# Kernel tuning notes

Measured on AMD Instinct MI355X. Metric: run time of the kernel, lower is better.

Reference implementation:

```python
import jax, jax.numpy as jnp
import numpy as np
import math

B, C, SEG, SEGLEN, K, GROUPS, WG = 8, 256, 40, 200, 10, 32, 4
L4 = SEGLEN // 4            # 50 temporal slots per segment
N = SEG * L4                # 2000 total points
WIDTH = GROUPS * WG         # 128 bottleneck width


def build_neighbor_idx(seg_lens):
    """Exact numpy replication of torch get_temporal_graph's neighbor-list loop.
    Returns flat (into B*N rows) neighbor indices of shape (B, N, 3)."""
    seg_lens = np.asarray(seg_lens)
    Bn, S = seg_lens.shape
    nb = np.zeros((Bn, S * L4, 3), dtype=np.int64)
    for i in range(Bn):
        last_valid = 0
        skip_seg = 0
        base = i * S * L4
        for j in range(S):
            valid = math.ceil(seg_lens[i, j] / 4.0)
            for k in range(L4):
                idx = j * L4 + k
                if k < valid:
                    nb[i, idx] = [base + last_valid, base + idx, base + idx]
                    last_valid = idx
                    if k == 0 and j != 0:
                        nb[i, skip_seg, 2] = base + idx
                    if k == valid - 1:
                        skip_seg = idx
                    else:
                        nb[i, idx, 2] = base + idx + 1
                else:
                    nb[i, idx] = [base + idx] * 3
    return nb


def conv1x1(x, W, b):
    # x: (B, Cin, N, T), W: (Cout, Cin)
    return jnp.einsum('bcnt,oc->bont', x, W) + b[None, :, None, None]


def grouped_1x3(x, W, b):
    # x: (B, WIDTH, N, 3), W: (WIDTH, WIDTH//GROUPS, 3); valid conv -> T_out = 1
    Bn, _, Nn, _ = x.shape
    xg = x.reshape(Bn, GROUPS, WIDTH // GROUPS, Nn, 3)
    Wg = W.reshape(GROUPS, WIDTH // GROUPS, WIDTH // GROUPS, 3)
    y = jnp.einsum('bgcnt,goct->bgon', xg, Wg)
    return y.reshape(Bn, WIDTH, Nn, 1) + b[None, :, None, None]


def grouped_1x1(x, W, b):
    # x: (B, WIDTH, N, T), W: (WIDTH, WIDTH//GROUPS)
    Bn, _, Nn, T = x.shape
    xg = x.reshape(Bn, GROUPS, WIDTH // GROUPS, Nn, T)
    Wg = W.reshape(GROUPS, WIDTH // GROUPS, WIDTH // GROUPS)
    y = jnp.einsum('bgcnt,goc->bgont', xg, Wg)
    return y.reshape(Bn, WIDTH, Nn, T) + b[None, :, None, None]


def setup_inputs() -> dict:
    key = jax.random.key(0)
    ks = jax.random.split(key, 10)
    s = 0.05
    x = jax.random.normal(ks[0], (B, C, N), dtype=jnp.float32)
    seg_lens = jax.random.randint(ks[1], (B, SEG), 0, 201)
    neighbor_idx = jnp.asarray(build_neighbor_idx(np.asarray(seg_lens)))
    return dict(
        x=x, seg_lens=seg_lens, neighbor_idx=neighbor_idx,
        tW1=jax.random.normal(ks[2], (WIDTH, C), jnp.float32) * s,
        tb1=jnp.zeros((WIDTH,), jnp.float32),
        tW2=jax.random.normal(ks[3], (WIDTH, WIDTH // GROUPS, 3), jnp.float32) * s,
        tb2=jnp.zeros((WIDTH,), jnp.float32),
        tW3=jax.random.normal(ks[4], (C, WIDTH), jnp.float32) * s,
        tb3=jnp.zeros((C,), jnp.float32),
        sW1=jax.random.normal(ks[5], (WIDTH, 2 * C), jnp.float32) * s,
        sb1=jnp.zeros((WIDTH,), jnp.float32),
        sW2=jax.random.normal(ks[6], (WIDTH, WIDTH // GROUPS), jnp.float32) * s,
        sb2=jnp.zeros((WIDTH,), jnp.float32),
        sW3=jax.random.normal(ks[7], (C, WIDTH), jnp.float32) * s,
        sb3=jnp.zeros((C,), jnp.float32),
    )


def reference(x, seg_lens, neighbor_idx, tW1, tb1, tW2, tb2, tW3, tb3,
              sW1, sb1, sW2, sb2, sW3, sb3):
    relu = jax.nn.relu
    B_, C_, N_ = x.shape
    flat = x.transpose(0, 2, 1).reshape(B_ * N_, C_)  # (B*N, C)

    # --- temporal branch: gather 3 temporal-graph neighbors -> (B, C, N, 3) ---
    tg = flat[neighbor_idx.reshape(-1)].reshape(B_, N_, 3, C_).transpose(0, 3, 1, 2)
    h = relu(conv1x1(tg, tW1, tb1))
    h = relu(grouped_1x3(h, tW2, tb2))
    tout = conv1x1(h, tW3, tb3).max(axis=-1)  # (B, C, N)

    # --- semantic branch: kNN graph feature (style=1) ---
    xx = jnp.sum(x * x, axis=1)                       # (B, N)
    inner = jnp.einsum('bci,bcj->bij', x, x)          # (B, N, N)
    pd = 2.0 * inner - xx[:, None, :] - xx[:, :, None]  # negative sq. distances
    _, idx = jax.lax.top_k(pd, K)                     # (B, N, K)
    base = (jnp.arange(B_) * N_)[:, None, None]
    nbr = flat[(idx + base).reshape(-1)].reshape(B_, N_, K, C_)
    center = jnp.broadcast_to(x.transpose(0, 2, 1)[:, :, None, :], (B_, N_, K, C_))
    xf = jnp.concatenate([nbr, center], axis=3).transpose(0, 3, 1, 2)  # (B, 2C, N, K)
    g = relu(conv1x1(xf, sW1, sb1))
    g = relu(grouped_1x1(g, sW2, sb2))
    sout = conv1x1(g, sW3, sb3).max(axis=-1)  # (B, C, N)

    return relu(tout + x + sout)
```

## Files before the change

kernel.cpp:

```cpp
#include <hip/hip_runtime.h>

#define NPTS 2000
#define NBATCH 8
#define NC 256
#define NW 128
#define NK 10
#define NROWS (NBATCH * NPTS)
#define JPAD 2048

typedef _Float16 f16x8 __attribute__((ext_vector_type(8)));
typedef _Float16 f16x4 __attribute__((ext_vector_type(4)));
typedef float f32x4 __attribute__((ext_vector_type(4)));

__device__ __forceinline__ float dot4(float4 a, float4 b) {
    return a.x*b.x + a.y*b.y + a.z*b.z + a.w*b.w;
}
__device__ __forceinline__ float4 relu4(float4 a) {
    return make_float4(fmaxf(a.x,0.f), fmaxf(a.y,0.f), fmaxf(a.z,0.f), fmaxf(a.w,0.f));
}
__device__ __forceinline__ float4 add4(float4 a, float4 b) {
    return make_float4(a.x+b.x, a.y+b.y, a.z+b.z, a.w+b.w);
}

__device__ __forceinline__ void ins10(float d, int j, float* vals, int* idxs) {
    if (d > vals[9]) {
        float v = d; int id = j;
        #pragma unroll
        for (int s = 0; s < 10; ++s) {
            if (v > vals[s]) {
                float tv = vals[s]; vals[s] = v; v = tv;
                int   ti = idxs[s]; idxs[s] = id; id = ti;
            }
        }
    }
}

__global__ __launch_bounds__(256) void k_prep(
    const float* __restrict__ x, _Float16* __restrict__ xb,
    float* __restrict__ xx)
{
    __shared__ float T[64][259];
    __shared__ float Pp[64][4];
    const int t  = threadIdx.x;
    const int b  = blockIdx.x >> 5;
    const int n0 = (blockIdx.x & 31) * 64;

    #pragma unroll
    for (int p = 0; p < 64; ++p) {
        const int idx = p*256 + t;
        const int c = idx >> 6, nl = idx & 63;
        T[nl][c] = x[((size_t)b*NC + c)*NPTS + min(n0 + nl, NPTS-1)];
    }
    __syncthreads();

    const int row = t & 63, q = t >> 6;
    const int gr  = n0 + row;
    const bool ok = gr < NPTS;
    const size_t rb = ((size_t)b*JPAD + gr) * 512;
    float ss = 0.f;
    #pragma unroll
    for (int u = 0; u < 2; ++u) {
        const int kc = 2*q + u;
        #pragma unroll
        for (int g = 0; g < 4; ++g) {
            f16x8 vh, vl;
            #pragma unroll
            for (int e = 0; e < 8; ++e) {
                const float f = ok ? T[row][kc*32 + g*8 + e] : 0.f;
                ss = fmaf(f, f, ss);
                const _Float16 h = (_Float16)f;
                vh[e] = h;
                vl[e] = (_Float16)(f - (float)h);
            }
            *(f16x8*)&xb[rb + (kc*2    )*32 + g*8] = vh;
            *(f16x8*)&xb[rb + (kc*2 + 1)*32 + g*8] = vl;
        }
    }
    Pp[row][q] = ss;
    __syncthreads();
    if (t < 64 && n0 + t < NPTS)
        xx[(size_t)b*NPTS + n0 + t] = Pp[t][0] + Pp[t][1] + Pp[t][2] + Pp[t][3];
}

__global__ __launch_bounds__(256) void k_wprep(const float* __restrict__ a,
                                               _Float16* __restrict__ o, int n)
{
    const int i = (blockIdx.x*256 + threadIdx.x)*4;
    if (i < n) {
        const float4 v = *(const float4*)&a[i];
        f16x4 h = {(_Float16)v.x, (_Float16)v.y, (_Float16)v.z, (_Float16)v.w};
        *(f16x4*)&o[i] = h;
    }
}

__global__ __launch_bounds__(256) void k_wcat(
    const float* __restrict__ tW1, const float* __restrict__ sW1,
    _Float16* __restrict__ whcat)
{
    const int idx = blockIdx.x*256 + threadIdx.x;
    const int n = idx >> 8, k = idx & 255;
    float v;
    if (n < 128)      v = tW1[n*256 + k];
    else if (n < 256) v = sW1[(n-128)*512 + k];
    else              v = sW1[(n-256)*512 + 256 + k];
    whcat[idx] = (_Float16)v;
}

__global__ __launch_bounds__(256) void k_rowmm(
    const _Float16* __restrict__ xb, const _Float16* __restrict__ whcat,
    const float* __restrict__ tb1, const float* __restrict__ sb1,
    float* __restrict__ T1r, float* __restrict__ P, float* __restrict__ Q)
{
    const int t = threadIdx.x, lane = t & 63, w = t >> 6;
    const int lr = lane & 15, rg = lane >> 4;
    const int r0 = blockIdx.x * 16;
    const int b  = r0 / NPTS, jr = r0 % NPTS;

    f16x8 ah[8], al[8];
    const size_t rb = ((size_t)b*JPAD + jr + lr) * 512 + rg*8;
    #pragma unroll
    for (int kc = 0; kc < 8; ++kc) {
        ah[kc] = *(const f16x8*)&xb[rb + kc*64];
        al[kc] = *(const f16x8*)&xb[rb + kc*64 + 32];
    }

    #pragma unroll
    for (int nt = 0; nt < 6; ++nt) {
        const int n0 = (w*6 + nt) * 16;
        f32x4 acc = {0.f,0.f,0.f,0.f};
        #pragma unroll
        for (int kc = 0; kc < 8; ++kc) {
            const f16x8 bw = *(const f16x8*)&whcat[(size_t)(n0 + lr)*256 + kc*32 + rg*8];
            acc = __builtin_amdgcn_mfma_f32_16x16x32_f16(ah[kc], bw, acc, 0,0,0);
            acc = __builtin_amdgcn_mfma_f32_16x16x32_f16(al[kc], bw, acc, 0,0,0);
        }
        const int n = n0 + lr;
        float bias; bool dorelu; float* dst;
        if (n < 128)      { bias = tb1[n];     dorelu = true;  dst = T1r + (size_t)r0*NW + n; }
        else if (n < 256) { bias = 0.f;        dorelu = false; dst = P   + (size_t)r0*NW + (n-128); }
        else              { bias = sb1[n-256]; dorelu = false; dst = Q   + (size_t)r0*NW + (n-256); }
        #pragma unroll
        for (int q = 0; q < 4; ++q) {
            float v = acc[q] + bias;
            if (dorelu) v = fmaxf(v, 0.f);
            dst[(size_t)(rg*4 + q)*NW] = v;
        }
    }
}

__global__ __launch_bounds__(256, 2) void k_topk(
    const _Float16* __restrict__ xb, const float* __restrict__ xx,
    float* __restrict__ pval, int* __restrict__ pidx)
{
    __shared__ __align__(16) char smem[20480];
    float* xxs = (float*)smem;

    const int t    = threadIdx.x;
    const int b    = blockIdx.x & 7;
    const int ig   = (blockIdx.x >> 3) & 31;
    const int jh   = blockIdx.x >> 8;
    const int i0   = ig * 64;
    const int lane = t & 63;
    const int w    = t >> 6;
    const int lr   = lane & 15, rg = lane >> 4;
    const size_t bj = (size_t)b * JPAD;
    const int tile0  = jh * 63;
    const int ntiles = jh ? 62 : 63;

    {
        const int cnt = ntiles * 16;
        for (int idx = t; idx < cnt; idx += 256)
            xxs[idx] = xx[(size_t)b*NPTS + tile0*16 + idx];
    }

    f16x8 bh[8], bl[8];
    {
        const int i = min(i0 + w*16 + lr, NPTS - 1);
        const size_t rb = (bj + i) * 512 + rg*8;
        #pragma unroll
        for (int kc = 0; kc < 8; ++kc) {
            bh[kc] = *(const f16x8*)&xb[rb + kc*64];
            bl[kc] = *(const f16x8*)&xb[rb + kc*64 + 32];
        }
    }

    float vals[10]; int idxs[10];
    #pragma unroll
    for (int s = 0; s < 10; ++s) { vals[s] = -3.0e38f; idxs[s] = 0x7fffffff; }

    __syncthreads();

    f16x8 RA[16], RB[16];
    const size_t lbase = (bj + lr) * 512 + rg*8;

#define LOADT(R, tt) { \
    const size_t a_ = lbase + (size_t)(tile0 + (tt)) * 8192; \
    _Pragma("unroll") \
    for (int p = 0; p < 16; ++p) R[p] = *(const f16x8*)&xb[a_ + p*32]; }

#define COMPUTE(R, tt) { \
    f32x4 acc = {0.f,0.f,0.f,0.f}; \
    _Pragma("unroll") \
    for (int kc = 0; kc < 8; ++kc) { \
        acc = __builtin_amdgcn_mfma_f32_16x16x32_f16(R[kc*2],   bh[kc], acc, 0,0,0); \
        acc = __builtin_amdgcn_mfma_f32_16x16x32_f16(R[kc*2],   bl[kc], acc, 0,0,0); \
        acc = __builtin_amdgcn_mfma_f32_16x16x32_f16(R[kc*2+1], bh[kc], acc, 0,0,0); \
    } \
    const int jr_ = (tt)*16 + rg*4; \
    const f32x4 xv_ = *(const f32x4*)&xxs[jr_]; \
    const float d0_ = 2.f*acc[0] - xv_[0]; \
    const float d1_ = 2.f*acc[1] - xv_[1]; \
    const float d2_ = 2.f*acc[2] - xv_[2]; \
    const float d3_ = 2.f*acc[3] - xv_[3]; \
    if (fmaxf(fmaxf(d0_,d1_), fmaxf(d2_,d3_)) > vals[9]) { \
        const int jg_ = (tile0 + (tt))*16 + rg*4; \
        ins10(d0_, jg_,     vals, idxs); \
        ins10(d1_, jg_ + 1, vals, idxs); \
        ins10(d2_, jg_ + 2, vals, idxs); \
        ins10(d3_, jg_ + 3, vals, idxs); } }

    LOADT(RA, 0)
    int jt = 0;
    while (jt + 2 <= ntiles) {
        LOADT(RB, jt + 1)
        COMPUTE(RA, jt)
        if (jt + 2 < ntiles) LOADT(RA, jt + 2)
        COMPUTE(RB, jt + 1)
        jt += 2;
    }
    if (jt < ntiles) COMPUTE(RA, jt)

#undef LOADT
#undef COMPUTE

    __syncthreads();
    float* mval = (float*)smem;
    int*   midx = (int*)(smem + 10240);
    {
        const int g = w*16 + lr;
        #pragma unroll
        for (int s = 0; s < 10; ++s) {
            mval[(g*4 + rg)*10 + s] = vals[s];
            midx[(g*4 + rg)*10 + s] = idxs[s];
        }
    }
    __syncthreads();
    if (t < 128) {
        const int g = t >> 1, pr = t & 1;
        float* va = &mval[(g*4 + pr)*10];     int* ia = &midx[(g*4 + pr)*10];
        const float* vb = &mval[(g*4 + pr + 2)*10]; const int* ib = &midx[(g*4 + pr + 2)*10];
        float ov[10]; int oi[10]; int pa = 0, pb = 0;
        #pragma unroll
        for (int s = 0; s < 10; ++s) {
            const float A = va[pa], Bv = vb[pb];
            const int  Ai = ia[pa], Bi = ib[pb];
            const bool ta = (A > Bv) || (A == Bv && Ai < Bi);
            ov[s] = ta ? A : Bv; oi[s] = ta ? Ai : Bi;
            pa += ta ? 1 : 0; pb += ta ? 0 : 1;
        }
        #pragma unroll
        for (int s = 0; s < 10; ++s) { va[s] = ov[s]; ia[s] = oi[s]; }
    }
    __syncthreads();
    if (t < 64) {
        const int g = t;
        const int i = i0 + g;
        if (i < NPTS) {
            const float* va = &mval[(g*4 + 0)*10]; const int* ia = &midx[(g*4 + 0)*10];
            const float* vb = &mval[(g*4 + 1)*10]; const int* ib = &midx[(g*4 + 1)*10];
            float* ov = &pval[((size_t)(b*NPTS + i)*2 + jh)*10];
            int*   oi = &pidx[((size_t)(b*NPTS + i)*2 + jh)*10];
            int pa = 0, pb = 0;
            #pragma unroll
            for (int s = 0; s < 10; ++s) {
                const float A = va[pa], Bv = vb[pb];
                const int  Ai = ia[pa], Bi = ib[pb];
                const bool ta = (A > Bv) || (A == Bv && Ai < Bi);
                ov[s] = ta ? A : Bv; oi[s] = ta ? Ai : Bi;
                pa += ta ? 1 : 0; pb += ta ? 0 : 1;
            }
        }
    }
}

__global__ __launch_bounds__(256) void k_tkmerge(
    const float* __restrict__ pval, const int* __restrict__ pidx,
    int* __restrict__ tk)
{
    const int r = blockIdx.x*256 + threadIdx.x;
    if (r >= NROWS) return;
    const float* va = &pval[(size_t)r*20];
    const int*   ia = &pidx[(size_t)r*20];
    const float* vb = va + 10;
    const int*   ib = ia + 10;
    const int base = (r / NPTS) * NPTS;
    int* op = &tk[(size_t)r*NK];
    int pa = 0, pb = 0;
    #pragma unroll
    for (int s = 0; s < NK; ++s) {
        const float A = va[pa], Bv = vb[pb];
        const int  Ai = ia[pa], Bi = ib[pb];
        const bool ta = (A > Bv) || (A == Bv && Ai < Bi);
        op[s] = base + (ta ? Ai : Bi);
        pa += ta ? 1 : 0; pb += ta ? 0 : 1;
    }
}

#define AST 136
__global__ __launch_bounds__(256, 2) void k_fused(
    const float* __restrict__ x,
    const int* __restrict__ nb, const int* __restrict__ tk,
    const float* __restrict__ T1r, const float* __restrict__ P, const float* __restrict__ Q,
    const float* __restrict__ tW2, const float* __restrict__ tb2,
    const float* __restrict__ sW2, const float* __restrict__ sb2,
    const _Float16* __restrict__ wt3h, const _Float16* __restrict__ ws3h,
    const float* __restrict__ tb3, const float* __restrict__ sb3,
    float* __restrict__ out)
{
    __shared__ __align__(16) _Float16 A16[144*AST];
    __shared__ float Ssm[8][260];
    __shared__ float Zr[8][260];

    const int t  = threadIdx.x;
    const int r0 = blockIdx.x * 8;
    const int bb = r0 / NPTS;
    const int n0 = r0 % NPTS;

    {
        const float4 z4 = make_float4(0.f,0.f,0.f,0.f);
        float4* p4 = (float4*)A16;
        #pragma unroll
        for (int i = 0; i < 10; ++i) {
            const int idx = t + i*256;
            if (idx < 2448) p4[idx] = z4;
        }
    }
    __syncthreads();

    {
        const int o    = t & 127;
        const int half = t >> 7;
        const int g4   = o & ~3;

        const float4 f0 = *(const float4*)&tW2[o*12];
        const float4 f1 = *(const float4*)&tW2[o*12 + 4];
        const float4 f2 = *(const float4*)&tW2[o*12 + 8];
        const float4 wt0 = make_float4(f0.x, f0.w, f1.z, f2.y);
        const float4 wt1 = make_float4(f0.y, f1.x, f1.w, f2.z);
        const float4 wt2 = make_float4(f0.z, f1.y, f2.x, f2.w);
        const float4 wsw = *(const float4*)&sW2[o*4];
        const float tb2o = tb2[o], sb2o = sb2[o];

        #pragma unroll
        for (int ptl = 0; ptl < 4; ++ptl) {
            const int pt = half*4 + ptl;
            const int r  = r0 + pt;
            const int nb0 = nb[r*3+0], nb1 = nb[r*3+1], nb2 = nb[r*3+2];
            int ki[NK];
            #pragma unroll
            for (int k = 0; k < NK; ++k) ki[k] = tk[r*NK + k];
            const float4 h0 = *(const float4*)&T1r[(size_t)nb0*NW + g4];
            const float4 h1 = *(const float4*)&T1r[(size_t)nb1*NW + g4];
            const float4 h2 = *(const float4*)&T1r[(size_t)nb2*NW + g4];
            const float4 qf = *(const float4*)&Q[(size_t)r*NW + g4];
            float4 pf[NK];
            #pragma unroll
            for (int k = 0; k < NK; ++k) pf[k] = *(const float4*)&P[(size_t)ki[k]*NW + g4];

            const float z = tb2o + dot4(wt0,h0) + dot4(wt1,h1) + dot4(wt2,h2);
            A16[(128 + pt)*AST + o] = (_Float16)fmaxf(z, 0.f);
            #pragma unroll
            for (int k = 0; k < NK; ++k) {
                const float4 g1 = relu4(add4(pf[k], qf));
                A16[(pt*16 + k)*AST + o] = (_Float16)fmaxf(dot4(wsw, g1) + sb2o, 0.f);
            }
        }
    }
    __syncthreads();

    const int lane = t & 63, w = t >> 6;
    const int lr = lane & 15, lg = lane >> 4;
    const int n0w = w * 64;

    f32x4 accG[8][4] = {};
    f32x4 accZ[4] = {};

    #pragma unroll
    for (int kt = 0; kt < 4; ++kt) {
        const int ko = kt*32 + lg*8;
        f16x8 bs[4], bt[4];
        #pragma unroll
        for (int nt = 0; nt < 4; ++nt) {
            const int n = n0w + nt*16 + lr;
            bs[nt] = *(const f16x8*)&ws3h[n*NW + ko];
            bt[nt] = *(const f16x8*)&wt3h[n*NW + ko];
        }
        #pragma unroll
        for (int mt = 0; mt < 8; ++mt) {
            const f16x8 a = *(const f16x8*)&A16[(mt*16 + lr)*AST + ko];
            #pragma unroll
            for (int nt = 0; nt < 4; ++nt)
                accG[mt][nt] = __builtin_amdgcn_mfma_f32_16x16x32_f16(a, bs[nt], accG[mt][nt], 0,0,0);
        }
        const f16x8 az = *(const f16x8*)&A16[(128 + lr)*AST + ko];
        #pragma unroll
        for (int nt = 0; nt < 4; ++nt)
            accZ[nt] = __builtin_amdgcn_mfma_f32_16x16x32_f16(az, bt[nt], accZ[nt], 0,0,0);
    }

    const int rg = lg;
    #pragma unroll
    for (int mt = 0; mt < 8; ++mt) {
        #pragma unroll
        for (int nt = 0; nt < 4; ++nt) {
            float v;
            if (rg < 2)       v = fmaxf(fmaxf(accG[mt][nt][0], accG[mt][nt][1]),
                                        fmaxf(accG[mt][nt][2], accG[mt][nt][3]));
            else if (rg == 2) v = fmaxf(accG[mt][nt][0], accG[mt][nt][1]);
            else              v = -3.0e38f;
            v = fmaxf(v, __shfl_xor(v, 16));
            v = fmaxf(v, __shfl_xor(v, 32));
            if (lane < 16) Ssm[mt][n0w + nt*16 + lane] = v;
        }
    }
    #pragma unroll
    for (int nt = 0; nt < 4; ++nt) {
        #pragma unroll
        for (int q = 0; q < 4; ++q) {
            if (rg < 2) Zr[rg*4 + q][n0w + nt*16 + lr] = accZ[nt][q];
        }
    }
    __syncthreads();

    {
        const int c = t;
        const float tb = tb3[c], sb = sb3[c];
        const size_t go = ((size_t)bb*NC + c)*NPTS + n0;
        const float4 xv0 = *(const float4*)&x[go];
        const float4 xv1 = *(const float4*)&x[go + 4];
        const float xr[8] = {xv0.x,xv0.y,xv0.z,xv0.w, xv1.x,xv1.y,xv1.z,xv1.w};
        float ov[8];
        #pragma unroll
        for (int p = 0; p < 8; ++p)
            ov[p] = fmaxf(Zr[p][c] + tb + Ssm[p][c] + sb + xr[p], 0.f);
        *(float4*)&out[go]     = make_float4(ov[0],ov[1],ov[2],ov[3]);
        *(float4*)&out[go + 4] = make_float4(ov[4],ov[5],ov[6],ov[7]);
    }
}

extern "C" void kernel_launch(void* const* d_in, const int* in_sizes, int n_in,
                              void* d_out, int out_size, void* d_ws, size_t ws_size,
                              hipStream_t stream) {
    (void)in_sizes; (void)n_in; (void)out_size; (void)ws_size;
    const float* x   = (const float*)d_in[0];
    const int*   nb  = (const int*)d_in[2];
    const float* tW1 = (const float*)d_in[3];
    const float* tb1 = (const float*)d_in[4];
    const float* tW2 = (const float*)d_in[5];
    const float* tb2 = (const float*)d_in[6];
    const float* tW3 = (const float*)d_in[7];
    const float* tb3 = (const float*)d_in[8];
    const float* sW1 = (const float*)d_in[9];
    const float* sb1 = (const float*)d_in[10];
    const float* sW2 = (const float*)d_in[11];
    const float* sb2 = (const float*)d_in[12];
    const float* sW3 = (const float*)d_in[13];
    const float* sb3 = (const float*)d_in[14];
    float* out = (float*)d_out;

    float* ws  = (float*)d_ws;
    float* T1r  = ws;
    float* P    = ws + 2048000;
    float* Q    = ws + 4096000;
    float* xxp  = ws + 6144000;
    int*   tk   = (int*)(ws + 6160000);
    float* pval = ws + 6320000;
    int*   pidx = (int*)(ws + 6640000);
    _Float16* xb    = (_Float16*)(ws + 6960000);
    _Float16* whcat = xb + (size_t)NBATCH * JPAD * 512;
    _Float16* wt3h  = whcat + 384 * 256;
    _Float16* ws3h  = wt3h + NC * NW;

    k_prep<<<NBATCH * 32, 256, 0, stream>>>(x, xb, xxp);
    k_wcat<<<384, 256, 0, stream>>>(tW1, sW1, whcat);
    k_wprep<<<32, 256, 0, stream>>>(tW3, wt3h, NC * NW);
    k_wprep<<<32, 256, 0, stream>>>(sW3, ws3h, NC * NW);
    k_rowmm<<<NROWS / 16, 256, 0, stream>>>(xb, whcat, tb1, sb1, T1r, P, Q);
    k_topk<<<512, 256, 0, stream>>>(xb, xxp, pval, pidx);
    k_tkmerge<<<(NROWS + 255) / 256, 256, 0, stream>>>(pval, pidx, tk);
    k_fused<<<NROWS / 8, 256, 0, stream>>>(x, nb, tk, T1r, P, Q,
                                           tW2, tb2, sW2, sb2, wt3h, ws3h, tb3, sb3, out);
}
```

Before: 392.7 us.

## Restructure kNN top-k as LDS-tiled MFMA GEMM with swizzled panel layout

The split-f16 xb buffer is re-laid out as per-k-chunk panels with an XOR swizzle, so rows can be streamed into LDS with global_load_lds double buffering. Each top-k block now covers 128 query rows and a quarter of the columns, keeping a 2x8 grid of accumulators so every loaded tile feeds more MFMAs. Before, each wave read its j tiles straight from global memory. The j range is split four ways instead of two, and the merge kernel now does a 4-way merge. The cost is more registers, a larger shared-memory footprint and extra partial-result storage.

```diff
diff --git a/kernel.cpp b/kernel.cpp
--- a/kernel.cpp
+++ b/kernel.cpp
@@ -35,6 +35,12 @@
     }
 }
 
+__device__ __forceinline__ void gl_lds16(const void* g, void* l) {
+    __builtin_amdgcn_global_load_lds(
+        (const __attribute__((address_space(1))) void*)g,
+        (__attribute__((address_space(3))) void*)l, 16, 0, 0);
+}
+
 __global__ __launch_bounds__(256) void k_prep(
     const float* __restrict__ x, _Float16* __restrict__ xb,
     float* __restrict__ xx)
@@ -56,11 +62,12 @@
     const int row = t & 63, q = t >> 6;
     const int gr  = n0 + row;
     const bool ok = gr < NPTS;
-    const size_t rb = ((size_t)b*JPAD + gr) * 512;
+    const int sx  = gr & 7;
     float ss = 0.f;
     #pragma unroll
     for (int u = 0; u < 2; ++u) {
         const int kc = 2*q + u;
+        const size_t base = ((size_t)(b*8 + kc)*JPAD + gr) * 64;
         #pragma unroll
         for (int g = 0; g < 4; ++g) {
             f16x8 vh, vl;
@@ -72,8 +79,8 @@
                 vh[e] = h;
                 vl[e] = (_Float16)(f - (float)h);
             }
-            *(f16x8*)&xb[rb + (kc*2    )*32 + g*8] = vh;
-            *(f16x8*)&xb[rb + (kc*2 + 1)*32 + g*8] = vl;
+            *(f16x8*)&xb[base + (size_t)((g     ^ sx))*8] = vh;
+            *(f16x8*)&xb[base + (size_t)(((4|g) ^ sx))*8] = vl;
         }
     }
     Pp[row][q] = ss;
@@ -116,12 +123,14 @@
     const int r0 = blockIdx.x * 16;
     const int b  = r0 / NPTS, jr = r0 % NPTS;
 
+    const int row = jr + lr;
+    const int sx  = row & 7;
     f16x8 ah[8], al[8];
-    const size_t rb = ((size_t)b*JPAD + jr + lr) * 512 + rg*8;
     #pragma unroll
     for (int kc = 0; kc < 8; ++kc) {
-        ah[kc] = *(const f16x8*)&xb[rb + kc*64];
-        al[kc] = *(const f16x8*)&xb[rb + kc*64 + 32];
+        const size_t base = ((size_t)(b*8 + kc)*JPAD + row) * 64;
+        ah[kc] = *(const f16x8*)&xb[base + (size_t)((rg     ^ sx))*8];
+        al[kc] = *(const f16x8*)&xb[base + (size_t)(((4|rg) ^ sx))*8];
     }
 
     #pragma unroll
@@ -152,100 +161,128 @@
     const _Float16* __restrict__ xb, const float* __restrict__ xx,
     float* __restrict__ pval, int* __restrict__ pidx)
 {
-    __shared__ __align__(16) char smem[20480];
-    float* xxs = (float*)smem;
+    __shared__ __align__(16) char smem[65536];
 
     const int t    = threadIdx.x;
     const int b    = blockIdx.x & 7;
-    const int ig   = (blockIdx.x >> 3) & 31;
-    const int jh   = blockIdx.x >> 8;
-    const int i0   = ig * 64;
+    const int ip   = (blockIdx.x >> 3) & 15;
+    const int j4   = blockIdx.x >> 7;
+    const int i0   = ip * 128;
     const int lane = t & 63;
     const int w    = t >> 6;
     const int lr   = lane & 15, rg = lane >> 4;
-    const size_t bj = (size_t)b * JPAD;
-    const int tile0  = jh * 63;
-    const int ntiles = jh ? 62 : 63;
+    const char* xbb = (const char*)xb;
+    const float* xxb = xx + (size_t)b * NPTS;
+
+    f32x4 acc[2][8] = {};
+    float v0[10], v1[10]; int x0[10], x1[10];
+    #pragma unroll
+    for (int s = 0; s < 10; ++s) { v0[s]=v1[s]=-3.0e38f; x0[s]=x1[s]=0x7fffffff; }
 
     {
-        const int cnt = ntiles * 16;
-        for (int idx = t; idx < cnt; idx += 256)
-            xxs[idx] = xx[(size_t)b*NPTS + tile0*16 + idx];
-    }
-
-    f16x8 bh[8], bl[8];
+        const size_t gbase = (size_t)(b*8 + 0) * JPAD;
+        const char* gi = xbb + (gbase + i0) * 128;
+        const char* gj = xbb + (gbase + (size_t)(j4*4 + 0)*128) * 128;
+        #pragma unroll
+        for (int r2 = 0; r2 < 4; ++r2) {
+            gl_lds16(gi + t*16 + r2*4096, smem + t*16 + r2*4096);
+            gl_lds16(gj + t*16 + r2*4096, smem + 16384 + t*16 + r2*4096);
+        }
+    }
+    __syncthreads();
+
+    for (int step = 0; step < 32; ++step) {
+        const int kc = step & 7, buf = step & 1, panel = step >> 3;
+
+        if (step < 31) {
+            const int ns = step + 1, nkc = ns & 7, npan = ns >> 3;
+            const size_t gbase = (size_t)(b*8 + nkc) * JPAD;
+            const char* gi = xbb + (gbase + i0) * 128;
+            const char* gj = xbb + (gbase + (size_t)(j4*4 + npan)*128) * 128;
+            char* li = smem + (buf ^ 1)*32768;
+            #pragma unroll
+            for (int r2 = 0; r2 < 4; ++r2) {
+                gl_lds16(gi + t*16 + r2*4096, li + t*16 + r2*4096);
+                gl_lds16(gj + t*16 + r2*4096, li + 16384 + t*16 + r2*4096);
+            }
+        }
+
+        {
+            const char* IB = smem + buf*32768;
+            const char* JB = IB + 16384;
+            f16x8 bhf[2], blf[2];
+            #pragma unroll
+            for (int it = 0; it < 2; ++it) {
+                const int il = (w*2 + it)*16 + lr;
+                const int sx = il & 7;
+                bhf[it] = *(const f16x8*)(IB + il*128 + ((rg     ^ sx))*16);
+                blf[it] = *(const f16x8*)(IB + il*128 + (((4|rg) ^ sx))*16);
+            }
+            #pragma unroll
+            for (int jt = 0; jt < 8; ++jt) {
+                const int jl = jt*16 + lr;
+                const int sx = jl & 7;
+                const f16x8 ajh = *(const f16x8*)(JB + jl*128 + ((rg     ^ sx))*16);
+                const f16x8 ajl = *(const f16x8*)(JB + jl*128 + (((4|rg) ^ sx))*16);
+                #pragma unroll
+                for (int it = 0; it < 2; ++it) {
+                    acc[it][jt] = __builtin_amdgcn_mfma_f32_16x16x32_f16(ajh, bhf[it], acc[it][jt], 0,0,0);
+                    acc[it][jt] = __builtin_amdgcn_mfma_f32_16x16x32_f16(ajh, blf[it], acc[it][jt], 0,0,0);
+                    acc[it][jt] = __builtin_amdgcn_mfma_f32_16x16x32_f16(ajl, bhf[it], acc[it][jt], 0,0,0);
+                }
+            }
+        }
+
+        if (kc == 7) {
+            const int jpan = (j4*4 + panel)*128;
+            #pragma unroll
+            for (int jt = 0; jt < 8; ++jt) {
+                const int jg0 = jpan + jt*16 + rg*4;
+                const f32x4 xv = *(const f32x4*)&xxb[min(jg0, NPTS-4)];
+                {
+                    const float d0 = 2.f*acc[0][jt][0] - xv[0];
+                    const float d1 = 2.f*acc[0][jt][1] - xv[1];
+                    const float d2 = 2.f*acc[0][jt][2] - xv[2];
+                    const float d3 = 2.f*acc[0][jt][3] - xv[3];
+                    if (fmaxf(fmaxf(d0,d1), fmaxf(d2,d3)) > v0[9]) {
+                        if (jg0     < NPTS) ins10(d0, jg0,     v0, x0);
+                        if (jg0 + 1 < NPTS) ins10(d1, jg0 + 1, v0, x0);
+                        if (jg0 + 2 < NPTS) ins10(d2, jg0 + 2, v0, x0);
+                        if (jg0 + 3 < NPTS) ins10(d3, jg0 + 3, v0, x0);
+                    }
+                    acc[0][jt] = (f32x4){0.f,0.f,0.f,0.f};
+                }
+                {
+                    const float d0 = 2.f*acc[1][jt][0] - xv[0];
+                    const float d1 = 2.f*acc[1][jt][1] - xv[1];
+                    const float d2 = 2.f*acc[1][jt][2] - xv[2];
+                    const float d3 = 2.f*acc[1][jt][3] - xv[3];
+                    if (fmaxf(fmaxf(d0,d1), fmaxf(d2,d3)) > v1[9]) {
+                        if (jg0     < NPTS) ins10(d0, jg0,     v1, x1);
+                        if (jg0 + 1 < NPTS) ins10(d1, jg0 + 1, v1, x1);
+                        if (jg0 + 2 < NPTS) ins10(d2, jg0 + 2, v1, x1);
+                        if (jg0 + 3 < NPTS) ins10(d3, jg0 + 3, v1, x1);
+                    }
+                    acc[1][jt] = (f32x4){0.f,0.f,0.f,0.f};
+                }
+            }
+        }
+        __syncthreads();
+    }
+
+    float* mval = (float*)smem;
+    int*   midx = (int*)(smem + 20480);
     {
-        const int i = min(i0 + w*16 + lr, NPTS - 1);
-        const size_t rb = (bj + i) * 512 + rg*8;
-        #pragma unroll
-        for (int kc = 0; kc < 8; ++kc) {
-            bh[kc] = *(const f16x8*)&xb[rb + kc*64];
-            bl[kc] = *(const f16x8*)&xb[rb + kc*64 + 32];
-        }
-    }
-
-    float vals[10]; int idxs[10];
-    #pragma unroll
-    for (int s = 0; s < 10; ++s) { vals[s] = -3.0e38f; idxs[s] = 0x7fffffff; }
-
-    __syncthreads();
-
-    f16x8 RA[16], RB[16];
-    const size_t lbase = (bj + lr) * 512 + rg*8;
-
-#define LOADT(R, tt) { \
-    const size_t a_ = lbase + (size_t)(tile0 + (tt)) * 8192; \
-    _Pragma("unroll") \
-    for (int p = 0; p < 16; ++p) R[p] = *(const f16x8*)&xb[a_ + p*32]; }
-
-#define COMPUTE(R, tt) { \
-    f32x4 acc = {0.f,0.f,0.f,0.f}; \
-    _Pragma("unroll") \
-    for (int kc = 0; kc < 8; ++kc) { \
-        acc = __builtin_amdgcn_mfma_f32_16x16x32_f16(R[kc*2],   bh[kc], acc, 0,0,0); \
-        acc = __builtin_amdgcn_mfma_f32_16x16x32_f16(R[kc*2],   bl[kc], acc, 0,0,0); \
-        acc = __builtin_amdgcn_mfma_f32_16x16x32_f16(R[kc*2+1], bh[kc], acc, 0,0,0); \
-    } \
-    const int jr_ = (tt)*16 + rg*4; \
-    const f32x4 xv_ = *(const f32x4*)&xxs[jr_]; \
-    const float d0_ = 2.f*acc[0] - xv_[0]; \
-    const float d1_ = 2.f*acc[1] - xv_[1]; \
-    const float d2_ = 2.f*acc[2] - xv_[2]; \
-    const float d3_ = 2.f*acc[3] - xv_[3]; \
-    if (fmaxf(fmaxf(d0_,d1_), fmaxf(d2_,d3_)) > vals[9]) { \
-        const int jg_ = (tile0 + (tt))*16 + rg*4; \
-        ins10(d0_, jg_,     vals, idxs); \
-        ins10(d1_, jg_ + 1, vals, idxs); \
-        ins10(d2_, jg_ + 2, vals, idxs); \
-        ins10(d3_, jg_ + 3, vals, idxs); } }
-
-    LOADT(RA, 0)
-    int jt = 0;
-    while (jt + 2 <= ntiles) {
-        LOADT(RB, jt + 1)
-        COMPUTE(RA, jt)
-        if (jt + 2 < ntiles) LOADT(RA, jt + 2)
-        COMPUTE(RB, jt + 1)
-        jt += 2;
-    }
-    if (jt < ntiles) COMPUTE(RA, jt)
-
-#undef LOADT
-#undef COMPUTE
-
-    __syncthreads();
-    float* mval = (float*)smem;
-    int*   midx = (int*)(smem + 10240);
+        const int g0 = (w*2 + 0)*16 + lr;
+        const int g1 = (w*2 + 1)*16 + lr;
+        #pragma unroll
+        for (int s = 0; s < 10; ++s) {
+            mval[(g0*4 + rg)*10 + s] = v0[s];  midx[(g0*4 + rg)*10 + s] = x0[s];
+            mval[(g1*4 + rg)*10 + s] = v1[s];  midx[(g1*4 + rg)*10 + s] = x1[s];
+        }
+    }
+    __syncthreads();
     {
-        const int g = w*16 + lr;
-        #pragma unroll
-        for (int s = 0; s < 10; ++s) {
-            mval[(g*4 + rg)*10 + s] = vals[s];
-            midx[(g*4 + rg)*10 + s] = idxs[s];
-        }
-    }
-    __syncthreads();
-    if (t < 128) {
         const int g = t >> 1, pr = t & 1;
         float* va = &mval[(g*4 + pr)*10];     int* ia = &midx[(g*4 + pr)*10];
         const float* vb = &mval[(g*4 + pr + 2)*10]; const int* ib = &midx[(g*4 + pr + 2)*10];
@@ -262,14 +299,14 @@
         for (int s = 0; s < 10; ++s) { va[s] = ov[s]; ia[s] = oi[s]; }
     }
     __syncthreads();
-    if (t < 64) {
+    if (t < 128) {
         const int g = t;
-        const int i = i0 + g;
-        if (i < NPTS) {
+        const int ig = i0 + g;
+        if (ig < NPTS) {
             const float* va = &mval[(g*4 + 0)*10]; const int* ia = &midx[(g*4 + 0)*10];
             const float* vb = &mval[(g*4 + 1)*10]; const int* ib = &midx[(g*4 + 1)*10];
-            float* ov = &pval[((size_t)(b*NPTS + i)*2 + jh)*10];
-            int*   oi = &pidx[((size_t)(b*NPTS + i)*2 + jh)*10];
+            float* ov = &pval[((size_t)(b*NPTS + ig)*4 + j4)*10];
+            int*   oi = &pidx[((size_t)(b*NPTS + ig)*4 + j4)*10];
             int pa = 0, pb = 0;
             #pragma unroll
             for (int s = 0; s < 10; ++s) {
@@ -289,20 +326,32 @@
 {
     const int r = blockIdx.x*256 + threadIdx.x;
     if (r >= NROWS) return;
-    const float* va = &pval[(size_t)r*20];
-    const int*   ia = &pidx[(size_t)r*20];
-    const float* vb = va + 10;
-    const int*   ib = ia + 10;
+    const float* v  = &pval[(size_t)r*40];
+    const int*   ix = &pidx[(size_t)r*40];
     const int base = (r / NPTS) * NPTS;
     int* op = &tk[(size_t)r*NK];
-    int pa = 0, pb = 0;
+    int p0 = 0, p1 = 0, p2 = 0, p3 = 0;
     #pragma unroll
     for (int s = 0; s < NK; ++s) {
-        const float A = va[pa], Bv = vb[pb];
-        const int  Ai = ia[pa], Bi = ib[pb];
-        const bool ta = (A > Bv) || (A == Bv && Ai < Bi);
-        op[s] = base + (ta ? Ai : Bi);
-        pa += ta ? 1 : 0; pb += ta ? 0 : 1;
+        float bv = -3.4e38f; int bi = 0x7fffffff; int bl = 0;
+        {
+            const float vv = v[p0];       const int ii = ix[p0];
+            if (vv > bv || (vv == bv && ii < bi)) { bv = vv; bi = ii; bl = 0; }
+        }
+        {
+            const float vv = v[10 + p1];  const int ii = ix[10 + p1];
+            if (vv > bv || (vv == bv && ii < bi)) { bv = vv; bi = ii; bl = 1; }
+        }
+        {
+            const float vv = v[20 + p2];  const int ii = ix[20 + p2];
+            if (vv > bv || (vv == bv && ii < bi)) { bv = vv; bi = ii; bl = 2; }
+        }
+        {
+            const float vv = v[30 + p3];  const int ii = ix[30 + p3];
+            if (vv > bv || (vv == bv && ii < bi)) { bv = vv; bi = ii; bl = 3; }
+        }
+        p0 += (bl == 0); p1 += (bl == 1); p2 += (bl == 2); p3 += (bl == 3);
+        op[s] = base + bi;
     }
 }
 
@@ -475,9 +524,9 @@
     float* xxp  = ws + 6144000;
     int*   tk   = (int*)(ws + 6160000);
     float* pval = ws + 6320000;
-    int*   pidx = (int*)(ws + 6640000);
-    _Float16* xb    = (_Float16*)(ws + 6960000);
-    _Float16* whcat = xb + (size_t)NBATCH * JPAD * 512;
+    int*   pidx = (int*)(ws + 6960000);
+    _Float16* xb    = (_Float16*)(ws + 7600000);
+    _Float16* whcat = xb + (size_t)NBATCH * 8 * JPAD * 64;
     _Float16* wt3h  = whcat + 384 * 256;
     _Float16* ws3h  = wt3h + NC * NW;
 
```

New measurement: 372.4 us. 5.2% less time.
